# Performance work log

Hardware: AMD Instinct MI355X
Metric: run time of the kernel (lower is better)

## Reference

```python
import jax, jax.numpy as jnp
import numpy as np

C = 256
HEADS = 8
HEAD_DIM = C // HEADS  # 32
B, H, W = 8, 128, 128


def conv1x1(x, w, b):
    # x: [B, Cin, H, W], w: [Cout, Cin], b: [Cout]
    return jnp.einsum('bchw,oc->bohw', x, w) + b[None, :, None, None]


def setup_inputs() -> dict:
    key = jax.random.key(0)
    ks = jax.random.split(key, 9)
    s = 1.0 / np.sqrt(C)  # conv1x1 fan-in init scale
    return {
        'x': jax.random.normal(ks[0], (B, C, H, W), dtype=jnp.float32),
        'wq': jax.random.normal(ks[1], (C, C), dtype=jnp.float32) * s,
        'bq': jax.random.normal(ks[2], (C,), dtype=jnp.float32) * s,
        'wk': jax.random.normal(ks[3], (C, C), dtype=jnp.float32) * s,
        'bk': jax.random.normal(ks[4], (C,), dtype=jnp.float32) * s,
        'wv': jax.random.normal(ks[5], (C, C), dtype=jnp.float32) * s,
        'bv': jax.random.normal(ks[6], (C,), dtype=jnp.float32) * s,
        'wo': jax.random.normal(ks[7], (C, C), dtype=jnp.float32) * s,
        'bo': jax.random.normal(ks[8], (C,), dtype=jnp.float32) * s,
    }


def reference(x, wq, bq, wk, bk, wv, bv, wo, bo):
    b, _, h, w = x.shape
    # [B, C, H, W] -> [B, heads, head_dim, H, W] -> transpose(1,2) -> [B, head_dim, heads, H, W]
    def split_heads(t):
        return t.reshape(b, HEADS, HEAD_DIM, h, w).swapaxes(1, 2)

    q = split_heads(conv1x1(x, wq, bq))
    k = split_heads(conv1x1(x, wk, bk))
    v = split_heads(conv1x1(x, wv, bv))

    q = q * (HEAD_DIM ** -0.25)  # only query is scaled, by head_dim**(1/4)
    # attention over rows H, contracting the W axis (faithful to the torch code)
    attn = jnp.einsum('bdnxw,bdnyw->bdnxy', q, k)       # [B, hd, heads, H, H]
    attn = jax.nn.softmax(attn, axis=-1)
    out = jnp.einsum('bdnxy,bdnyw->bdnxw', attn, v)     # [B, hd, heads, H, W]

    out = out.swapaxes(1, 2).reshape(b, C, h, w)        # back to [B, C, H, W]
    return conv1x1(out, wo, bo)
```

## Files before the change

kernel.cpp:

```cpp
#include <hip/hip_runtime.h>
#include <hip/hip_bf16.h>
#include <stdint.h>

#define CDIM 256
#define HDIM 128
#define WDIM 128
#define HW   (HDIM * WDIM)
#define BATCH 8
#define BUFE  ((size_t)BATCH * CDIM * HW)

typedef __bf16 bf16;
typedef bf16  bf16x8 __attribute__((ext_vector_type(8)));
typedef float f32x4  __attribute__((ext_vector_type(4)));

#define MFMA16(a, b, c) __builtin_amdgcn_mfma_f32_16x16x32_bf16((a), (b), (c), 0, 0, 0)


__device__ __forceinline__ bf16x8 read_afrag(const bf16* As, int ROWelems, int row, int kelem) {
    const char* base = (const char*)As;
    int cb = (kelem * 2) ^ ((row & 7) << 4);
    return *reinterpret_cast<const bf16x8*>(base + row * ROWelems * 2 + cb);
}

__device__ __forceinline__ void write_a16B(bf16* As, int ROWelems, int row, int colbytes, bf16x8 v) {
    char* base = (char*)As;
    *reinterpret_cast<bf16x8*>(base + row * ROWelems * 2 + (colbytes ^ ((row & 7) << 4))) = v;
}

__device__ __forceinline__ int bsub_idx(int k, int n) {
    return (((k >> 2) << 3) + (n >> 4)) * 64 + ((k & 3) << 4) + (n & 15);
}

__device__ __forceinline__ bf16x8 read_bfrag(const bf16* Bs, int kbase, int ntile, int lane) {
    int g = lane >> 4;
    int n = (ntile << 4) + (lane & 15);
    int k0 = kbase + (g << 3);
    bf16x8 r;
#pragma unroll
    for (int j = 0; j < 8; ++j) {
        r[j] = Bs[bsub_idx(k0 + j, n)];
    }
    return r;
}

__device__ __forceinline__ bf16x8 cvt8(float4 a, float4 b) {
    bf16x8 v;
    v[0] = (bf16)a.x; v[1] = (bf16)a.y; v[2] = (bf16)a.z; v[3] = (bf16)a.w;
    v[4] = (bf16)b.x; v[5] = (bf16)b.y; v[6] = (bf16)b.z; v[7] = (bf16)b.w;
    return v;
}

__global__ __launch_bounds__(512) void proj_kernel(
    const float* __restrict__ x,
    const float* __restrict__ wq, const float* __restrict__ bq,
    const float* __restrict__ wk, const float* __restrict__ bk,
    const float* __restrict__ wv, const float* __restrict__ bv,
    bf16* __restrict__ qkv)
{
    int pt = blockIdx.x;
    int z  = blockIdx.y;
    int b = z / 3, m = z - 3 * b;
    const float* Wm = (m == 0) ? wq : (m == 1) ? wk : wv;
    const float* Bm = (m == 0) ? bq : (m == 1) ? bk : bv;
    const float* xb = x + (size_t)b * CDIM * HW;
    bf16* outb = qkv + (size_t)m * BUFE + (size_t)b * CDIM * HW;
    int p0 = pt * 128;

    __shared__ bf16 As[256 * 64];
    __shared__ bf16 Bs[64 * 128];

    int t = threadIdx.x;
    int wave = t >> 6, lane = t & 63;
    int wm = wave >> 1, wn = wave & 1;

    f32x4 acc[4][4];
#pragma unroll
    for (int i = 0; i < 4; ++i)
#pragma unroll
        for (int j = 0; j < 4; ++j) acc[i][j] = (f32x4){0.f, 0.f, 0.f, 0.f};

    for (int kk = 0; kk < CDIM; kk += 64) {
#pragma unroll
        for (int pass = 0; pass < 2; ++pass) {
            int row = pass * 128 + (t >> 2);
            int cbe = (t & 3) * 16;
            const float4* src = reinterpret_cast<const float4*>(Wm + row * CDIM + kk + cbe);
            float4 f0 = src[0], f1 = src[1], f2 = src[2], f3 = src[3];
            write_a16B(As, 64, row, cbe * 2,      cvt8(f0, f1));
            write_a16B(As, 64, row, cbe * 2 + 16, cvt8(f2, f3));
        }
        {
            int c  = t >> 3;
            int pb = (t & 7) * 16;
            const float4* src = reinterpret_cast<const float4*>(xb + (size_t)(kk + c) * HW + p0 + pb);
            float4 f0 = src[0], f1 = src[1], f2 = src[2], f3 = src[3];
            int idx = (((c >> 2) << 3) + (pb >> 4)) * 64 + ((c & 3) << 4);
            *reinterpret_cast<bf16x8*>(&Bs[idx])     = cvt8(f0, f1);
            *reinterpret_cast<bf16x8*>(&Bs[idx + 8]) = cvt8(f2, f3);
        }
        __syncthreads();
#pragma unroll
        for (int ks = 0; ks < 64; ks += 32) {
            int ke = ks + ((lane >> 4) << 3);
            bf16x8 af[4], bfr[4];
#pragma unroll
            for (int i = 0; i < 4; ++i)
                af[i] = read_afrag(As, 64, wm * 64 + i * 16 + (lane & 15), ke);
#pragma unroll
            for (int j = 0; j < 4; ++j)
                bfr[j] = read_bfrag(Bs, ks, wn * 4 + j, lane);
#pragma unroll
            for (int i = 0; i < 4; ++i)
#pragma unroll
                for (int j = 0; j < 4; ++j)
                    acc[i][j] = MFMA16(af[i], bfr[j], acc[i][j]);
        }
        __syncthreads();
    }
#pragma unroll
    for (int i = 0; i < 4; ++i) {
#pragma unroll
        for (int r = 0; r < 4; ++r) {
            int o = wm * 64 + i * 16 + ((lane >> 4) << 2) + r;
            float bias = Bm[o];
#pragma unroll
            for (int j = 0; j < 4; ++j) {
                int p = p0 + wn * 64 + j * 16 + (lane & 15);
                outb[(size_t)o * HW + p] = (bf16)(acc[i][j][r] + bias);
            }
        }
    }
}

__global__ __launch_bounds__(512) void attn_kernel(bf16* __restrict__ qkv)
{
    int bc = blockIdx.x;
    size_t blk = (size_t)bc * HW;
    bf16* qb       = qkv + blk;
    const bf16* kb = qkv + BUFE + blk;
    const bf16* vb = qkv + 2 * BUFE + blk;

    __shared__ bf16 Qs[128 * 128];
    __shared__ bf16 Ks[128 * 128];
    __shared__ bf16 Vs[128 * 128];
    __shared__ bf16 Ps[128 * 128];

    int t = threadIdx.x;
    int wave = t >> 6, lane = t & 63;

    {
        int row = t >> 2;
        int cb  = (t & 3) * 32;
        const uint4* qsrc = reinterpret_cast<const uint4*>(qb + (size_t)row * WDIM + cb);
        const uint4* ksrc = reinterpret_cast<const uint4*>(kb + (size_t)row * WDIM + cb);
        const uint4* vsrc = reinterpret_cast<const uint4*>(vb + (size_t)row * WDIM + cb);
        char* qdst = (char*)Qs + row * 256;
        char* kdst = (char*)Ks + row * 256;
        int sw = (row & 7) << 4;
#pragma unroll
        for (int u = 0; u < 4; ++u) {
            int off = cb * 2 + u * 16;
            *reinterpret_cast<uint4*>(qdst + (off ^ sw)) = qsrc[u];
            *reinterpret_cast<uint4*>(kdst + (off ^ sw)) = ksrc[u];
        }
#pragma unroll
        for (int u = 0; u < 4; ++u) {
            int e = cb + u * 8;
            int idx = (((row >> 2) << 3) + (e >> 4)) * 64 + ((row & 3) << 4) + (e & 8);
            *reinterpret_cast<uint4*>(&Vs[idx]) = vsrc[u];
        }
    }
    __syncthreads();

    f32x4 sacc[8];
#pragma unroll
    for (int j = 0; j < 8; ++j) sacc[j] = (f32x4){0.f, 0.f, 0.f, 0.f};
#pragma unroll
    for (int ks = 0; ks < 128; ks += 32) {
        int ke = ks + ((lane >> 4) << 3);
        bf16x8 aq = read_afrag(Qs, 128, (wave << 4) + (lane & 15), ke);
#pragma unroll
        for (int j = 0; j < 8; ++j) {
            bf16x8 bk8 = read_afrag(Ks, 128, (j << 4) + (lane & 15), ke);
            sacc[j] = MFMA16(aq, bk8, sacc[j]);
        }
    }

    const float SCALE_QK = 0.42044820762685725f;
    float rinv[4];
#pragma unroll
    for (int r = 0; r < 4; ++r) {
        float mx = -1e30f;
#pragma unroll
        for (int j = 0; j < 8; ++j) {
            sacc[j][r] *= SCALE_QK;
            mx = fmaxf(mx, sacc[j][r]);
        }
#pragma unroll
        for (int d = 1; d < 16; d <<= 1) mx = fmaxf(mx, __shfl_xor(mx, d));
        float sum = 0.f;
#pragma unroll
        for (int j = 0; j < 8; ++j) {
            float e = __expf(sacc[j][r] - mx);
            sacc[j][r] = e;
            sum += e;
        }
#pragma unroll
        for (int d = 1; d < 16; d <<= 1) sum += __shfl_xor(sum, d);
        rinv[r] = 1.0f / sum;
        int row = (wave << 4) + ((lane >> 4) << 2) + r;
        char* pdst = (char*)Ps + row * 256;
        int swp = (row & 7) << 4;
#pragma unroll
        for (int j = 0; j < 8; ++j) {
            int colb = ((j << 4) + (lane & 15)) * 2;
            *reinterpret_cast<bf16*>(pdst + (colb ^ swp)) = (bf16)sacc[j][r];
        }
    }

    f32x4 oacc[8];
#pragma unroll
    for (int j = 0; j < 8; ++j) oacc[j] = (f32x4){0.f, 0.f, 0.f, 0.f};
#pragma unroll
    for (int ks = 0; ks < 128; ks += 32) {
        int ke = ks + ((lane >> 4) << 3);
        bf16x8 ap = read_afrag(Ps, 128, (wave << 4) + (lane & 15), ke);
#pragma unroll
        for (int j = 0; j < 8; ++j) {
            bf16x8 bv8 = read_bfrag(Vs, ks, j, lane);
            oacc[j] = MFMA16(ap, bv8, oacc[j]);
        }
    }
#pragma unroll
    for (int r = 0; r < 4; ++r) {
        int xrow = (wave << 4) + ((lane >> 4) << 2) + r;
#pragma unroll
        for (int j = 0; j < 8; ++j) {
            qb[(size_t)xrow * WDIM + (j << 4) + (lane & 15)] = (bf16)(oacc[j][r] * rinv[r]);
        }
    }
}

__global__ __launch_bounds__(512) void outproj_kernel(
    const bf16* __restrict__ ao, const float* __restrict__ Wo,
    const float* __restrict__ bo, float* __restrict__ out)
{
    int pt = blockIdx.x, b = blockIdx.y;
    const bf16* aob = ao + (size_t)b * CDIM * HW;
    float* outb = out + (size_t)b * CDIM * HW;
    int p0 = pt * 128;

    __shared__ bf16 As[256 * 64];
    __shared__ bf16 Bs[64 * 128];

    int t = threadIdx.x;
    int wave = t >> 6, lane = t & 63;
    int wm = wave >> 1, wn = wave & 1;

    f32x4 acc[4][4];
#pragma unroll
    for (int i = 0; i < 4; ++i)
#pragma unroll
        for (int j = 0; j < 4; ++j) acc[i][j] = (f32x4){0.f, 0.f, 0.f, 0.f};

    for (int kk = 0; kk < CDIM; kk += 64) {
#pragma unroll
        for (int pass = 0; pass < 2; ++pass) {
            int row = pass * 128 + (t >> 2);
            int cbe = (t & 3) * 16;
            const float4* src = reinterpret_cast<const float4*>(Wo + row * CDIM + kk + cbe);
            float4 f0 = src[0], f1 = src[1], f2 = src[2], f3 = src[3];
            write_a16B(As, 64, row, cbe * 2,      cvt8(f0, f1));
            write_a16B(As, 64, row, cbe * 2 + 16, cvt8(f2, f3));
        }
        {
            int c  = t >> 3;
            int pb = (t & 7) * 16;
            const uint4* src = reinterpret_cast<const uint4*>(aob + (size_t)(kk + c) * HW + p0 + pb);
            uint4 v0 = src[0], v1 = src[1];
            int idx = (((c >> 2) << 3) + (pb >> 4)) * 64 + ((c & 3) << 4);
            *reinterpret_cast<uint4*>(&Bs[idx])     = v0;
            *reinterpret_cast<uint4*>(&Bs[idx + 8]) = v1;
        }
        __syncthreads();
#pragma unroll
        for (int ks = 0; ks < 64; ks += 32) {
            int ke = ks + ((lane >> 4) << 3);
            bf16x8 af[4], bfr[4];
#pragma unroll
            for (int i = 0; i < 4; ++i)
                af[i] = read_afrag(As, 64, wm * 64 + i * 16 + (lane & 15), ke);
#pragma unroll
            for (int j = 0; j < 4; ++j)
                bfr[j] = read_bfrag(Bs, ks, wn * 4 + j, lane);
#pragma unroll
            for (int i = 0; i < 4; ++i)
#pragma unroll
                for (int j = 0; j < 4; ++j)
                    acc[i][j] = MFMA16(af[i], bfr[j], acc[i][j]);
        }
        __syncthreads();
    }
#pragma unroll
    for (int i = 0; i < 4; ++i) {
#pragma unroll
        for (int r = 0; r < 4; ++r) {
            int o = wm * 64 + i * 16 + ((lane >> 4) << 2) + r;
            float bias = bo[o];
#pragma unroll
            for (int j = 0; j < 4; ++j) {
                int p = p0 + wn * 64 + j * 16 + (lane & 15);
                outb[(size_t)o * HW + p] = acc[i][j][r] + bias;
            }
        }
    }
}

extern "C" void kernel_launch(void* const* d_in, const int* in_sizes, int n_in,
                              void* d_out, int out_size, void* d_ws, size_t ws_size,
                              hipStream_t stream) {
    const float* x  = (const float*)d_in[0];
    const float* wq = (const float*)d_in[1];
    const float* bq = (const float*)d_in[2];
    const float* wk = (const float*)d_in[3];
    const float* bk = (const float*)d_in[4];
    const float* wv = (const float*)d_in[5];
    const float* bv = (const float*)d_in[6];
    const float* wo = (const float*)d_in[7];
    const float* bo = (const float*)d_in[8];
    float* out = (float*)d_out;
    bf16* qkv = (bf16*)d_ws;

    proj_kernel<<<dim3(128, 24), 512, 0, stream>>>(x, wq, bq, wk, bk, wv, bv, qkv);
    attn_kernel<<<dim3(2048), 512, 0, stream>>>(qkv);
    outproj_kernel<<<dim3(128, 8), 512, 0, stream>>>(qkv, wo, bo, out);
}
```

Baseline: 501.2 us.

## Transpose B operands into swizzled K-contiguous LDS tiles for vector fragment reads

The B-operand tiles in all three kernels (the x tile in the projection, V in attention, the attention output in the out-projection) are transposed in registers while being staged into shared memory. They are stored as row-per-N, K-contiguous tiles with an XOR swizzle, replacing the old sub-tiled layout that needed eight scalar 2-byte LDS reads per MFMA fragment. Each fragment becomes one 16-byte vector load, which cuts LDS instruction count in the inner loops. The cost is register shuffling and narrower 8-byte LDS writes during staging, plus global loads that now span four rows per thread.

```diff
diff --git a/kernel.cpp b/kernel.cpp
--- a/kernel.cpp
+++ b/kernel.cpp
@@ -11,6 +11,9 @@
 
 typedef __bf16 bf16;
 typedef bf16  bf16x8 __attribute__((ext_vector_type(8)));
+typedef bf16  bf16x4 __attribute__((ext_vector_type(4)));
+typedef unsigned short u16x4 __attribute__((ext_vector_type(4)));
+typedef unsigned short u16x8 __attribute__((ext_vector_type(8)));
 typedef float f32x4  __attribute__((ext_vector_type(4)));
 
 #define MFMA16(a, b, c) __builtin_amdgcn_mfma_f32_16x16x32_bf16((a), (b), (c), 0, 0, 0)
@@ -27,20 +30,17 @@
     *reinterpret_cast<bf16x8*>(base + row * ROWelems * 2 + (colbytes ^ ((row & 7) << 4))) = v;
 }
 
-__device__ __forceinline__ int bsub_idx(int k, int n) {
-    return (((k >> 2) << 3) + (n >> 4)) * 64 + ((k & 3) << 4) + (n & 15);
-}
-
-__device__ __forceinline__ bf16x8 read_bfrag(const bf16* Bs, int kbase, int ntile, int lane) {
-    int g = lane >> 4;
-    int n = (ntile << 4) + (lane & 15);
-    int k0 = kbase + (g << 3);
-    bf16x8 r;
-#pragma unroll
-    for (int j = 0; j < 8; ++j) {
-        r[j] = Bs[bsub_idx(k0 + j, n)];
-    }
-    return r;
+__device__ __forceinline__ int swt(int row) {
+    return ((row ^ (row >> 3)) & 7) << 4;
+}
+__device__ __forceinline__ bf16x8 read_tfrag(const bf16* Ts, int ROWelems, int row, int kelem) {
+    const char* base = (const char*)Ts;
+    int cb = (kelem * 2) ^ swt(row);
+    return *reinterpret_cast<const bf16x8*>(base + row * ROWelems * 2 + cb);
+}
+__device__ __forceinline__ void write_t8B(bf16* Ts, int ROWelems, int row, int colbytes, u16x4 v) {
+    char* base = (char*)Ts;
+    *reinterpret_cast<u16x4*>(base + row * ROWelems * 2 + (colbytes ^ swt(row))) = v;
 }
 
 __device__ __forceinline__ bf16x8 cvt8(float4 a, float4 b) {
@@ -48,6 +48,11 @@
     v[0] = (bf16)a.x; v[1] = (bf16)a.y; v[2] = (bf16)a.z; v[3] = (bf16)a.w;
     v[4] = (bf16)b.x; v[5] = (bf16)b.y; v[6] = (bf16)b.z; v[7] = (bf16)b.w;
     return v;
+}
+
+__device__ __forceinline__ unsigned short bfbits(float f) {
+    bf16 h = (bf16)f;
+    return __builtin_bit_cast(unsigned short, h);
 }
 
 __global__ __launch_bounds__(512) void proj_kernel(
@@ -67,7 +72,7 @@
     int p0 = pt * 128;
 
     __shared__ bf16 As[256 * 64];
-    __shared__ bf16 Bs[64 * 128];
+    __shared__ bf16 Bs[128 * 64];
 
     int t = threadIdx.x;
     int wave = t >> 6, lane = t & 63;
@@ -90,13 +95,22 @@
             write_a16B(As, 64, row, cbe * 2 + 16, cvt8(f2, f3));
         }
         {
-            int c  = t >> 3;
-            int pb = (t & 7) * 16;
-            const float4* src = reinterpret_cast<const float4*>(xb + (size_t)(kk + c) * HW + p0 + pb);
-            float4 f0 = src[0], f1 = src[1], f2 = src[2], f3 = src[3];
-            int idx = (((c >> 2) << 3) + (pb >> 4)) * 64 + ((c & 3) << 4);
-            *reinterpret_cast<bf16x8*>(&Bs[idx])     = cvt8(f0, f1);
-            *reinterpret_cast<bf16x8*>(&Bs[idx + 8]) = cvt8(f2, f3);
+            int pb = t & 31;
+            int cb = t >> 5;
+            int p = pb * 4, c = cb * 4;
+            float4 f[4];
+#pragma unroll
+            for (int r = 0; r < 4; ++r)
+                f[r] = *reinterpret_cast<const float4*>(xb + (size_t)(kk + c + r) * HW + p0 + p);
+#pragma unroll
+            for (int i = 0; i < 4; ++i) {
+                u16x4 v;
+                v[0] = bfbits(((const float*)&f[0])[i]);
+                v[1] = bfbits(((const float*)&f[1])[i]);
+                v[2] = bfbits(((const float*)&f[2])[i]);
+                v[3] = bfbits(((const float*)&f[3])[i]);
+                write_t8B(Bs, 64, p + i, c * 2, v);
+            }
         }
         __syncthreads();
 #pragma unroll
@@ -108,7 +122,7 @@
                 af[i] = read_afrag(As, 64, wm * 64 + i * 16 + (lane & 15), ke);
 #pragma unroll
             for (int j = 0; j < 4; ++j)
-                bfr[j] = read_bfrag(Bs, ks, wn * 4 + j, lane);
+                bfr[j] = read_tfrag(Bs, 64, wn * 64 + j * 16 + (lane & 15), ke);
 #pragma unroll
             for (int i = 0; i < 4; ++i)
 #pragma unroll
@@ -153,7 +167,6 @@
         int cb  = (t & 3) * 32;
         const uint4* qsrc = reinterpret_cast<const uint4*>(qb + (size_t)row * WDIM + cb);
         const uint4* ksrc = reinterpret_cast<const uint4*>(kb + (size_t)row * WDIM + cb);
-        const uint4* vsrc = reinterpret_cast<const uint4*>(vb + (size_t)row * WDIM + cb);
         char* qdst = (char*)Qs + row * 256;
         char* kdst = (char*)Ks + row * 256;
         int sw = (row & 7) << 4;
@@ -163,11 +176,20 @@
             *reinterpret_cast<uint4*>(qdst + (off ^ sw)) = qsrc[u];
             *reinterpret_cast<uint4*>(kdst + (off ^ sw)) = ksrc[u];
         }
-#pragma unroll
-        for (int u = 0; u < 4; ++u) {
-            int e = cb + u * 8;
-            int idx = (((row >> 2) << 3) + (e >> 4)) * 64 + ((row & 3) << 4) + (e & 8);
-            *reinterpret_cast<uint4*>(&Vs[idx]) = vsrc[u];
+    }
+    {
+        int yb = t & 31;
+        int wb = t >> 5;
+        int y0 = yb * 4, w0 = wb * 8;
+        u16x8 rv[4];
+#pragma unroll
+        for (int r = 0; r < 4; ++r)
+            rv[r] = *reinterpret_cast<const u16x8*>(vb + (size_t)(y0 + r) * WDIM + w0);
+#pragma unroll
+        for (int i = 0; i < 8; ++i) {
+            u16x4 v;
+            v[0] = rv[0][i]; v[1] = rv[1][i]; v[2] = rv[2][i]; v[3] = rv[3][i];
+            write_t8B(Vs, 128, w0 + i, y0 * 2, v);
         }
     }
     __syncthreads();
@@ -227,7 +249,7 @@
         bf16x8 ap = read_afrag(Ps, 128, (wave << 4) + (lane & 15), ke);
 #pragma unroll
         for (int j = 0; j < 8; ++j) {
-            bf16x8 bv8 = read_bfrag(Vs, ks, j, lane);
+            bf16x8 bv8 = read_tfrag(Vs, 128, (j << 4) + (lane & 15), ke);
             oacc[j] = MFMA16(ap, bv8, oacc[j]);
         }
     }
@@ -251,7 +273,7 @@
     int p0 = pt * 128;
 
     __shared__ bf16 As[256 * 64];
-    __shared__ bf16 Bs[64 * 128];
+    __shared__ bf16 Bs[128 * 64];
 
     int t = threadIdx.x;
     int wave = t >> 6, lane = t & 63;
@@ -274,13 +296,19 @@
             write_a16B(As, 64, row, cbe * 2 + 16, cvt8(f2, f3));
         }
         {
-            int c  = t >> 3;
-            int pb = (t & 7) * 16;
-            const uint4* src = reinterpret_cast<const uint4*>(aob + (size_t)(kk + c) * HW + p0 + pb);
-            uint4 v0 = src[0], v1 = src[1];
-            int idx = (((c >> 2) << 3) + (pb >> 4)) * 64 + ((c & 3) << 4);
-            *reinterpret_cast<uint4*>(&Bs[idx])     = v0;
-            *reinterpret_cast<uint4*>(&Bs[idx + 8]) = v1;
+            int pb = t & 31;
+            int cb = t >> 5;
+            int p = pb * 4, c = cb * 4;
+            u16x4 rv[4];
+#pragma unroll
+            for (int r = 0; r < 4; ++r)
+                rv[r] = *reinterpret_cast<const u16x4*>(aob + (size_t)(kk + c + r) * HW + p0 + p);
+#pragma unroll
+            for (int i = 0; i < 4; ++i) {
+                u16x4 v;
+                v[0] = rv[0][i]; v[1] = rv[1][i]; v[2] = rv[2][i]; v[3] = rv[3][i];
+                write_t8B(Bs, 64, p + i, c * 2, v);
+            }
         }
         __syncthreads();
 #pragma unroll
@@ -292,7 +320,7 @@
                 af[i] = read_afrag(As, 64, wm * 64 + i * 16 + (lane & 15), ke);
 #pragma unroll
             for (int j = 0; j < 4; ++j)
-                bfr[j] = read_bfrag(Bs, ks, wn * 4 + j, lane);
+                bfr[j] = read_tfrag(Bs, 64, wn * 64 + j * 16 + (lane & 15), ke);
 #pragma unroll
             for (int i = 0; i < 4; ++i)
 #pragma unroll
```

After: 488.8 us. -2.5%, faster.
